# Kernel optimization log

Hardware: AMD Instinct MI355X
Metric: run time of the kernel (lower is better)

Reference implementation:

```python
import jax, jax.numpy as jnp
import numpy as np

T = 64        # time steps (batch)
N_SIDE = 256  # grid side, N = N_SIDE**2 flattened grid points
HID = 32      # hidden width of the shared per-point MLP
IN_CH = 5     # 5-point periodic stencil (l, l2, center, r, r2)


def _stencil_gather(x, n):
    """Replicates MLPConv._preprocess / make_px / get_value exactly.

    x: [T, n*n] flattened periodic grid. Returns [T, n*n, 5].
    get_value wraps indices via the piecewise rule (v-n if v>=n) and relies on
    numpy negative flat indexing for v=-1, which is the final `% (n*n)` here.
    Output position i_loop*n + j_loop reads grid flat index (j_loop+ik) + n*(i_loop+jk).
    """
    ii = jnp.arange(n)[:, None]  # i_loop (outer loop in make_px)
    jj = jnp.arange(n)[None, :]  # j_loop (inner loop)

    def idx(ik, jk):
        a = jj + ik
        a = jnp.where(a >= n, a - n, a)
        b = ii + jk
        b = jnp.where(b >= n, b - n, b)
        return ((a + n * b) % (n * n)).reshape(-1)  # [n*n]

    # channel order from _preprocess: cat([l, l2, px, r, r2], -1)
    offsets = [(-1, 0), (0, -1), (0, 0), (1, 0), (0, 1)]
    cols = jnp.stack([idx(ik, jk) for ik, jk in offsets], axis=-1)  # [n*n, 5]
    return x[:, cols]  # [T, n*n, 5]


def setup_inputs() -> dict:
    key = jax.random.key(0)
    ks = jax.random.split(key, 7)
    n2 = N_SIDE * N_SIDE
    x = jax.random.normal(ks[0], (T, n2), dtype=jnp.float32)
    # torch Linear weights are [out, in]; we store transposed [in, out] for x @ W.
    # Original init: xavier_normal * 10, bias zeros; scaled normals are equivalent for a baseline.
    def w(k, fan_in, fan_out):
        std = 10.0 * np.sqrt(2.0 / (fan_in + fan_out))
        return std * jax.random.normal(k, (fan_in, fan_out), dtype=jnp.float32)
    return {
        "x": x,
        "W0": w(ks[1], IN_CH, HID), "b0": jnp.zeros((HID,), jnp.float32),
        "W1": w(ks[2], HID, HID),   "b1": jnp.zeros((HID,), jnp.float32),
        "W2": w(ks[3], HID, 1),     "b2": jnp.zeros((1,), jnp.float32),
    }


def reference(x, W0, b0, W1, b1, W2, b2):
    # Note: the x_copy dual path in the torch forward never affects the returned
    # tensor (dead code), so the faithful math is a plain 3-layer MLP over the
    # 5-point periodic stencil gather, ELU between layers, no final activation.
    n = int(np.sqrt(x.shape[1]))
    px = _stencil_gather(x, n)                 # [T, N, 5]
    h = jax.nn.elu(px @ W0 + b0)               # [T, N, HID]
    h = jax.nn.elu(h @ W1 + b1)                # [T, N, HID]
    out = h @ W2 + b2                          # [T, N, 1]
    return out.squeeze(-1)                     # [T, N] (matches res.squeeze())
```

## Files before the change

### kernel.cpp

```cpp
#include <hip/hip_runtime.h>
#include <hip/hip_fp16.h>

#define NS 256
#define N2 (NS * NS)
#define HID 32
#define T_STEPS 64

typedef _Float16 h2     __attribute__((ext_vector_type(2)));
typedef _Float16 half8  __attribute__((ext_vector_type(8)));
typedef float    float4v __attribute__((ext_vector_type(4)));

union H8 { half8 v8; h2 v2[4]; };

__device__ __forceinline__ h2 pk(float a, float b) {
    return __builtin_bit_cast(h2, __builtin_amdgcn_cvt_pkrtz(a, b));
}

__device__ __forceinline__ h2 elu2(h2 z) {
    h2 zero; zero[0] = (_Float16)0.f; zero[1] = (_Float16)0.f;
    h2 zm  = __builtin_elementwise_min(z, zero);
    h2 e   = __builtin_elementwise_exp2(zm * (_Float16)1.442695041f);
    h2 em1 = e + (_Float16)(-1.0f);
    return __builtin_elementwise_max(z, em1);
}

__global__ __launch_bounds__(256, 4) void mlpconv_3mfma_kernel(
    const float* __restrict__ x,
    const float* __restrict__ W0, const float* __restrict__ b0,
    const float* __restrict__ W1, const float* __restrict__ b1,
    const float* __restrict__ W2, const float* __restrict__ b2,
    float* __restrict__ out)
{
    const int lane = threadIdx.x & 63;
    const int m    = lane & 15;
    const int kg   = lane >> 4;

    const int c0 = 8 * (m >> 2) + (m & 3);
    const int c1 = c0 + 4;

    H8 a00, a01;
    #pragma unroll
    for (int i = 0; i < 8; ++i) {
        const int k = 8 * kg + i;
        a00.v8[i] = (k < 5) ? (_Float16)W0[k * HID + c0] : (_Float16)0.f;
        a01.v8[i] = (k < 5) ? (_Float16)W0[k * HID + c1] : (_Float16)0.f;
    }
    H8 a10, a11;
    #pragma unroll
    for (int i = 0; i < 8; ++i) {
        a10.v8[i] = (_Float16)W1[(8 * kg + i) * HID + c0];
        a11.v8[i] = (_Float16)W1[(8 * kg + i) * HID + c1];
    }
    H8 a2;
    #pragma unroll
    for (int i = 0; i < 8; ++i)
        a2.v8[i] = (m == 0) ? (_Float16)W2[8 * kg + i] : (_Float16)0.f;

    float4v cl0a, cl0b, cl1a, cl1b;
    #pragma unroll
    for (int r = 0; r < 4; ++r) {
        cl0a[r] = b0[8 * kg + r];
        cl0b[r] = b0[8 * kg + 4 + r];
        cl1a[r] = b1[8 * kg + r];
        cl1b[r] = b1[8 * kg + 4 + r];
    }
    float4v c2;
    c2[0] = (kg == 0) ? b2[0] : 0.0f;
    c2[1] = 0.0f; c2[2] = 0.0f; c2[3] = 0.0f;

    asm volatile("" : "+v"(a00.v8), "+v"(a01.v8), "+v"(a10.v8), "+v"(a11.v8),
                      "+v"(a2.v8), "+v"(cl0a), "+v"(cl0b), "+v"(cl1a), "+v"(cl1b));

    const int wid   = __builtin_amdgcn_readfirstlane(threadIdx.x >> 6);
    const int t     = blockIdx.y;
    const int i0    = blockIdx.x * 4 + wid;
    const int sbase = i0 << 8;

    const float* __restrict__ xt  = x + ((size_t)t << 16);
    const float* __restrict__ xtu = xt + ((i0 == 0)      ? (N2 - NS) : -NS);
    const float* __restrict__ xtd = xt + ((i0 == NS - 1) ? -(N2 - NS) : NS);
    float* __restrict__       ob  = out + ((size_t)t << 16);

    const unsigned vc0 = (unsigned)(sbase + m);
    const unsigned vl0 = (unsigned)(sbase + m - 1);
    const unsigned vlA = (sbase + m == 0) ? (unsigned)(N2 - 1) : vl0;
    const unsigned vr0 = (unsigned)(sbase + m + 1);
    const unsigned vrF = (m == 15) ? (unsigned)sbase : (vr0 + 240u);

    #pragma unroll
    for (int l = 0; l < 16; ++l) {
        const unsigned o = 16u * (unsigned)l;
        const float in0 = xt [(l == 0)  ? vlA : (vl0 + o)];
        const float in1 = xtu[vc0 + o];
        const float in2 = xt [vc0 + o];
        const float in3 = xt [(l == 15) ? vrF : (vr0 + o)];
        const float in4 = xtd[vc0 + o];

        H8 bf;
        bf.v2[0] = pk(in0, in1);
        bf.v2[1] = pk(in2, in3);
        bf.v2[2] = pk(in4, in4);
        bf.v2[3] = bf.v2[2];

        float4v d0 = __builtin_amdgcn_mfma_f32_16x16x32_f16(a00.v8, bf.v8, cl0a, 0, 0, 0);
        float4v d1 = __builtin_amdgcn_mfma_f32_16x16x32_f16(a01.v8, bf.v8, cl0b, 0, 0, 0);

        H8 hf;
        hf.v2[0] = elu2(pk(d0[0], d0[1]));
        hf.v2[1] = elu2(pk(d0[2], d0[3]));
        hf.v2[2] = elu2(pk(d1[0], d1[1]));
        hf.v2[3] = elu2(pk(d1[2], d1[3]));

        float4v e0 = __builtin_amdgcn_mfma_f32_16x16x32_f16(a10.v8, hf.v8, cl1a, 0, 0, 0);
        float4v e1 = __builtin_amdgcn_mfma_f32_16x16x32_f16(a11.v8, hf.v8, cl1b, 0, 0, 0);

        H8 gf;
        gf.v2[0] = elu2(pk(e0[0], e0[1]));
        gf.v2[1] = elu2(pk(e0[2], e0[3]));
        gf.v2[2] = elu2(pk(e1[0], e1[1]));
        gf.v2[3] = elu2(pk(e1[2], e1[3]));

        float4v dz = __builtin_amdgcn_mfma_f32_16x16x32_f16(a2.v8, gf.v8, c2, 0, 0, 0);

        if (kg == 0) ob[vc0 + o] = dz[0];
    }
}

extern "C" void kernel_launch(void* const* d_in, const int* in_sizes, int n_in,
                              void* d_out, int out_size, void* d_ws, size_t ws_size,
                              hipStream_t stream) {
    const float* x  = (const float*)d_in[0];
    const float* W0 = (const float*)d_in[1];
    const float* b0 = (const float*)d_in[2];
    const float* W1 = (const float*)d_in[3];
    const float* b1 = (const float*)d_in[4];
    const float* W2 = (const float*)d_in[5];
    const float* b2 = (const float*)d_in[6];
    float* out = (float*)d_out;

    dim3 grid(NS / 4, T_STEPS);
    mlpconv_3mfma_kernel<<<grid, dim3(256), 0, stream>>>(
        x, W0, b0, W1, b1, W2, b2, out);
}
```

Measured before the change: 127.3 us.

## Switch MLP to 32x32x16 MFMA tiles and batch all stencil loads upfront

```diff
diff --git a/kernel.cpp b/kernel.cpp
--- a/kernel.cpp
+++ b/kernel.cpp
@@ -6,9 +6,9 @@
 #define HID 32
 #define T_STEPS 64
 
-typedef _Float16 h2     __attribute__((ext_vector_type(2)));
-typedef _Float16 half8  __attribute__((ext_vector_type(8)));
-typedef float    float4v __attribute__((ext_vector_type(4)));
+typedef _Float16 h2      __attribute__((ext_vector_type(2)));
+typedef _Float16 half8   __attribute__((ext_vector_type(8)));
+typedef float    float16v __attribute__((ext_vector_type(16)));
 
 union H8 { half8 v8; h2 v2[4]; };
 
@@ -24,7 +24,7 @@
     return __builtin_elementwise_max(z, em1);
 }
 
-__global__ __launch_bounds__(256, 4) void mlpconv_3mfma_kernel(
+__global__ __launch_bounds__(256, 2) void mlpconv_3232_kernel(
     const float* __restrict__ x,
     const float* __restrict__ W0, const float* __restrict__ b0,
     const float* __restrict__ W1, const float* __restrict__ b1,
@@ -32,44 +32,38 @@
     float* __restrict__ out)
 {
     const int lane = threadIdx.x & 63;
-    const int m    = lane & 15;
-    const int kg   = lane >> 4;
+    const int c    = lane & 31;
+    const int h    = lane >> 5;
+    const int kb   = 8 * h;
 
-    const int c0 = 8 * (m >> 2) + (m & 3);
-    const int c1 = c0 + 4;
+    const int rr = c;
+    const int Pb = rr & 3, Ph = (rr >> 2) & 1, Pq = rr >> 3;
+    const int P  = 16 * (Pq >> 1) + 8 * Ph + 4 * (Pq & 1) + Pb;
 
-    H8 a00, a01;
+    H8 a0, a1a, a1b, a2a, a2b;
     #pragma unroll
     for (int i = 0; i < 8; ++i) {
-        const int k = 8 * kg + i;
-        a00.v8[i] = (k < 5) ? (_Float16)W0[k * HID + c0] : (_Float16)0.f;
-        a01.v8[i] = (k < 5) ? (_Float16)W0[k * HID + c1] : (_Float16)0.f;
+        const int k = kb + i;
+        a0.v8[i]  = (k < 5) ? (_Float16)W0[k * HID + P] : (_Float16)0.f;
+        a1a.v8[i] = (_Float16)W1[k * HID + P];
+        a1b.v8[i] = (_Float16)W1[(16 + k) * HID + P];
+        a2a.v8[i] = (rr == 0) ? (_Float16)W2[k]      : (_Float16)0.f;
+        a2b.v8[i] = (rr == 0) ? (_Float16)W2[16 + k] : (_Float16)0.f;
     }
-    H8 a10, a11;
+
+    float16v c0i, c1i, c2i;
     #pragma unroll
-    for (int i = 0; i < 8; ++i) {
-        a10.v8[i] = (_Float16)W1[(8 * kg + i) * HID + c0];
-        a11.v8[i] = (_Float16)W1[(8 * kg + i) * HID + c1];
+    for (int reg = 0; reg < 16; ++reg) {
+        const int ch = (reg < 8) ? (8 * h + reg) : (16 + 8 * h + (reg - 8));
+        c0i[reg] = b0[ch];
+        c1i[reg] = b1[ch];
+        c2i[reg] = 0.0f;
     }
-    H8 a2;
-    #pragma unroll
-    for (int i = 0; i < 8; ++i)
-        a2.v8[i] = (m == 0) ? (_Float16)W2[8 * kg + i] : (_Float16)0.f;
+    if (h == 0) c2i[0] = b2[0];
 
-    float4v cl0a, cl0b, cl1a, cl1b;
-    #pragma unroll
-    for (int r = 0; r < 4; ++r) {
-        cl0a[r] = b0[8 * kg + r];
-        cl0b[r] = b0[8 * kg + 4 + r];
-        cl1a[r] = b1[8 * kg + r];
-        cl1b[r] = b1[8 * kg + 4 + r];
-    }
-    float4v c2;
-    c2[0] = (kg == 0) ? b2[0] : 0.0f;
-    c2[1] = 0.0f; c2[2] = 0.0f; c2[3] = 0.0f;
-
-    asm volatile("" : "+v"(a00.v8), "+v"(a01.v8), "+v"(a10.v8), "+v"(a11.v8),
-                      "+v"(a2.v8), "+v"(cl0a), "+v"(cl0b), "+v"(cl1a), "+v"(cl1b));
+    asm volatile("" : "+v"(a0.v8), "+v"(a1a.v8), "+v"(a1b.v8),
+                      "+v"(a2a.v8), "+v"(a2b.v8),
+                      "+v"(c0i), "+v"(c1i), "+v"(c2i));
 
     const int wid   = __builtin_amdgcn_readfirstlane(threadIdx.x >> 6);
     const int t     = blockIdx.y;
@@ -81,48 +75,64 @@
     const float* __restrict__ xtd = xt + ((i0 == NS - 1) ? -(N2 - NS) : NS);
     float* __restrict__       ob  = out + ((size_t)t << 16);
 
-    const unsigned vc0 = (unsigned)(sbase + m);
-    const unsigned vl0 = (unsigned)(sbase + m - 1);
-    const unsigned vlA = (sbase + m == 0) ? (unsigned)(N2 - 1) : vl0;
-    const unsigned vr0 = (unsigned)(sbase + m + 1);
-    const unsigned vrF = (m == 15) ? (unsigned)sbase : (vr0 + 240u);
+    const unsigned vc0 = (unsigned)(sbase + c);
+    const unsigned vl0 = (unsigned)(sbase + c - 1);
+    const unsigned vlA = (sbase + c == 0) ? (unsigned)(N2 - 1) : vl0;
+    const unsigned vr0 = (unsigned)(sbase + c + 1);
+    const unsigned vrF = (c == 31) ? (unsigned)sbase : (vr0 + 224u);
+
+    float in_[8][5];
+    #pragma unroll
+    for (int tl = 0; tl < 8; ++tl) {
+        const unsigned o = 32u * (unsigned)tl;
+        in_[tl][0] = xt [(tl == 0) ? vlA : (vl0 + o)];
+        in_[tl][1] = xtu[vc0 + o];
+        in_[tl][2] = xt [vc0 + o];
+        in_[tl][3] = xt [(tl == 7) ? vrF : (vr0 + o)];
+        in_[tl][4] = xtd[vc0 + o];
+    }
+
+    float res[8];
 
     #pragma unroll
-    for (int l = 0; l < 16; ++l) {
-        const unsigned o = 16u * (unsigned)l;
-        const float in0 = xt [(l == 0)  ? vlA : (vl0 + o)];
-        const float in1 = xtu[vc0 + o];
-        const float in2 = xt [vc0 + o];
-        const float in3 = xt [(l == 15) ? vrF : (vr0 + o)];
-        const float in4 = xtd[vc0 + o];
+    for (int tl = 0; tl < 8; ++tl) {
+        const float* s = in_[tl];
 
         H8 bf;
-        bf.v2[0] = pk(in0, in1);
-        bf.v2[1] = pk(in2, in3);
-        bf.v2[2] = pk(in4, in4);
+        bf.v2[0] = pk(s[0], s[1]);
+        bf.v2[1] = pk(s[2], s[3]);
+        bf.v2[2] = pk(s[4], s[4]);
         bf.v2[3] = bf.v2[2];
 
-        float4v d0 = __builtin_amdgcn_mfma_f32_16x16x32_f16(a00.v8, bf.v8, cl0a, 0, 0, 0);
-        float4v d1 = __builtin_amdgcn_mfma_f32_16x16x32_f16(a01.v8, bf.v8, cl0b, 0, 0, 0);
+        float16v d0 = __builtin_amdgcn_mfma_f32_32x32x16_f16(a0.v8, bf.v8, c0i, 0, 0, 0);
 
-        H8 hf;
-        hf.v2[0] = elu2(pk(d0[0], d0[1]));
-        hf.v2[1] = elu2(pk(d0[2], d0[3]));
-        hf.v2[2] = elu2(pk(d1[0], d1[1]));
-        hf.v2[3] = elu2(pk(d1[2], d1[3]));
+        H8 hf1, hf2;
+        #pragma unroll
+        for (int j = 0; j < 4; ++j) {
+            hf1.v2[j] = elu2(pk(d0[2 * j],     d0[2 * j + 1]));
+            hf2.v2[j] = elu2(pk(d0[8 + 2 * j], d0[8 + 2 * j + 1]));
+        }
 
-        float4v e0 = __builtin_amdgcn_mfma_f32_16x16x32_f16(a10.v8, hf.v8, cl1a, 0, 0, 0);
-        float4v e1 = __builtin_amdgcn_mfma_f32_16x16x32_f16(a11.v8, hf.v8, cl1b, 0, 0, 0);
+        float16v e = __builtin_amdgcn_mfma_f32_32x32x16_f16(a1a.v8, hf1.v8, c1i, 0, 0, 0);
+        e = __builtin_amdgcn_mfma_f32_32x32x16_f16(a1b.v8, hf2.v8, e, 0, 0, 0);
 
-        H8 gf;
-        gf.v2[0] = elu2(pk(e0[0], e0[1]));
-        gf.v2[1] = elu2(pk(e0[2], e0[3]));
-        gf.v2[2] = elu2(pk(e1[0], e1[1]));
-        gf.v2[3] = elu2(pk(e1[2], e1[3]));
+        H8 gf1, gf2;
+        #pragma unroll
+        for (int j = 0; j < 4; ++j) {
+            gf1.v2[j] = elu2(pk(e[2 * j],     e[2 * j + 1]));
+            gf2.v2[j] = elu2(pk(e[8 + 2 * j], e[8 + 2 * j + 1]));
+        }
 
-        float4v dz = __builtin_amdgcn_mfma_f32_16x16x32_f16(a2.v8, gf.v8, c2, 0, 0, 0);
+        float16v dz = __builtin_amdgcn_mfma_f32_32x32x16_f16(a2a.v8, gf1.v8, c2i, 0, 0, 0);
+        dz = __builtin_amdgcn_mfma_f32_32x32x16_f16(a2b.v8, gf2.v8, dz, 0, 0, 0);
 
-        if (kg == 0) ob[vc0 + o] = dz[0];
+        res[tl] = dz[0];
+    }
+
+    if (h == 0) {
+        #pragma unroll
+        for (int tl = 0; tl < 8; ++tl)
+            ob[vc0 + 32u * (unsigned)tl] = res[tl];
     }
 }
 
@@ -139,6 +149,6 @@
     float* out = (float*)d_out;
 
     dim3 grid(NS / 4, T_STEPS);
-    mlpconv_3mfma_kernel<<<grid, dim3(256), 0, stream>>>(
+    mlpconv_3232_kernel<<<grid, dim3(256), 0, stream>>>(
         x, W0, b0, W1, b1, W2, b2, out);
 }
```

Measured after the change: 124.4 us. 2.2% less time.
